# Kernel optimization log

Hardware: AMD Instinct MI355X
Metric: run time of the kernel (lower is better)

Reference implementation:

```python
import jax, jax.numpy as jnp
import numpy as np

BIGINT = 1e10

def sinusoidal_embed(pos, dim):
    # SinusoidalPositionEmbedding: interleaved sin/cos, matches torch reshape order
    idx = jnp.arange(dim // 2, dtype=jnp.float32)
    freq = jnp.power(10000.0, -2.0 * idx / dim)
    ang = pos.astype(jnp.float32)[:, None] * freq[None, :]          # [N, d/2]
    emb = jnp.stack([jnp.sin(ang), jnp.cos(ang)], axis=-1)          # [N, d/2, 2]
    return emb.reshape(pos.shape[0], dim)

def dihedral(a, b, c, d):
    # standard signed dihedral angle of four points, [...,3] -> [...]
    u1, u2, u3 = b - a, c - b, d - c
    n1 = jnp.cross(u1, u2)
    n2 = jnp.cross(u2, u3)
    u2n = u2 / (jnp.linalg.norm(u2, axis=-1, keepdims=True) + 1e-12)
    m = jnp.cross(n1, u2n)
    x = jnp.sum(n1 * n2, axis=-1)
    y = jnp.sum(m * n2, axis=-1)
    return jnp.arctan2(y, x)

def knn_edges(X, Seg, bid, k):
    # faithful dense formulation of _construct_knn: pairwise min-over-channel-pair
    # distance, masked by (same bid) & (same Seg), then smallest-k per row.
    N = X.shape[0]
    rule = (bid[:, None] == bid[None, :]) & (Seg[:, None] == Seg[None, :])  # [N,N]
    sq = jnp.sum(X * X, axis=-1)                                   # [N,C]
    dot = jnp.einsum('icd,jed->icje', X, X)                        # [N,C,N,C]
    d2 = sq[:, :, None, None] + sq[None, None, :, :] - 2.0 * dot   # [N,C,N,C]
    dmin = jnp.sqrt(jnp.maximum(jnp.min(d2, axis=(1, 3)), 0.0))    # [N,N]
    dist = jnp.where(rule, dmin, BIGINT)
    neg_vals, dst = jax.lax.top_k(-dist, k)                        # smallest-k
    dnb = -neg_vals                                                # [N,k]
    src = jnp.broadcast_to(jnp.arange(N)[:, None], (N, k))
    valid = (dnb < BIGINT).reshape(-1)                             # [N*k]
    dst = dst.reshape(-1)
    src = src.reshape(-1)
    # torch compacts invalid edges (dynamic shape); we pad them with -1 + mask
    edges = jnp.stack([jnp.where(valid, dst, -1), jnp.where(valid, src, -1)])
    return edges, valid

def pairwise_dihedrals(X, dst, src):
    # inter-residue dihedrals on backbone atoms, channels = [N, CA, C, O]
    ir_phi = dihedral(X[dst, 2], X[src, 0], X[src, 1], X[src, 2])  # C_i, N_j, CA_j, C_j
    ir_psi = dihedral(X[dst, 0], X[dst, 1], X[dst, 2], X[src, 0])  # N_i, CA_i, C_i, N_j
    return jnp.stack([ir_phi, ir_psi], axis=-1)                    # [E, 2]

def setup_inputs() -> dict:
    key = jax.random.key(0)
    ks = jax.random.split(key, 8)
    N, C, E, NUM_AA, NUM_ID = 3000, 4, 64, 21, 2
    X = jax.random.normal(ks[0], (N, C, 3), dtype=jnp.float32) * 10.0
    S = jax.random.randint(ks[1], (N,), 0, NUM_AA)
    RP = jax.random.randint(ks[2], (N,), 0, 1000)
    ID = jax.random.randint(ks[3], (N,), 0, NUM_ID)
    Seg = jax.random.randint(ks[4], (N,), 0, 2)
    bid = jnp.sort(jax.random.randint(ks[5], (N,), 0, 8))
    res_embed = jax.random.normal(ks[6], (NUM_AA, E), dtype=jnp.float32)
    id_embed = jax.random.normal(ks[7], (NUM_ID, E), dtype=jnp.float32)
    return {"X": X, "S": S, "RP": RP, "ID": ID, "Seg": Seg, "bid": bid,
            "res_embed": res_embed, "id_embed": id_embed, "k_neighbors": 10}

def reference(X, S, RP, ID, Seg, bid, res_embed, id_embed, k_neighbors):
    # node features: [residue embedding, positional + chain-id embedding]
    res_h = res_embed[S]                                           # [N,E]
    rp_h = sinusoidal_embed(RP, res_embed.shape[1]) + id_embed[ID] # [N,E]
    H = jnp.concatenate([res_h, rp_h], axis=-1)                    # [N,2E]
    edges, valid = knn_edges(X, Seg, bid, k_neighbors)             # [2,N*k], [N*k]
    dst = jnp.maximum(edges[0], 0)
    src = jnp.maximum(edges[1], 0)
    edge_attr = pairwise_dihedrals(X, dst, src)                    # [N*k,2]
    edge_attr = jnp.where(valid[:, None], edge_attr, 0.0)
    return H, edges, edge_attr, valid
```

## Files before the change

kernel.cpp:

```cpp
#include <hip/hip_runtime.h>
#include <math.h>

#define TOPK 10
#define WAVE 64
#define MAX_N 3072

__device__ __forceinline__ void cross3(const float* a, const float* b, float* o) {
    o[0] = a[1] * b[2] - a[2] * b[1];
    o[1] = a[2] * b[0] - a[0] * b[2];
    o[2] = a[0] * b[1] - a[1] * b[0];
}
__device__ __forceinline__ float dot3(const float* a, const float* b) {
    return a[0] * b[0] + a[1] * b[1] + a[2] * b[2];
}

__device__ float dihedral4(const float* a, const float* b, const float* c, const float* d) {
    float u1[3], u2[3], u3[3];
    #pragma unroll
    for (int t = 0; t < 3; t++) {
        u1[t] = b[t] - a[t];
        u2[t] = c[t] - b[t];
        u3[t] = d[t] - c[t];
    }
    float n1[3], n2[3];
    cross3(u1, u2, n1);
    cross3(u2, u3, n2);
    float nrm = sqrtf(dot3(u2, u2)) + 1e-12f;
    float u2n[3] = {u2[0] / nrm, u2[1] / nrm, u2[2] / nrm};
    float m[3];
    cross3(n1, u2n, m);
    float x = dot3(n1, n2);
    float y = dot3(m, n2);
    return atan2f(y, x);
}

__global__ void node_feat_kernel(const float* __restrict__ res_embed,
                                 const float* __restrict__ id_embed,
                                 const int* __restrict__ S,
                                 const int* __restrict__ RP,
                                 const int* __restrict__ ID,
                                 float* __restrict__ H,
                                 int N, int E) {
    int idx = blockIdx.x * blockDim.x + threadIdx.x;
    if (idx >= N * E) return;
    int n = idx / E;
    int e = idx - n * E;
    float* Hrow = H + (size_t)n * 2 * E;
    Hrow[e] = res_embed[S[n] * E + e];
    if (e < E / 2) {
        int half = e;
        float freq = powf(10000.0f, -2.0f * (float)half / (float)E);
        float ang = (float)RP[n] * freq;
        const float* idrow = id_embed + ID[n] * E;
        Hrow[E + 2 * half + 0] = sinf(ang) + idrow[2 * half + 0];
        Hrow[E + 2 * half + 1] = cosf(ang) + idrow[2 * half + 1];
    }
}

__global__ __launch_bounds__(WAVE) void knn_wave_kernel(
    const float* __restrict__ X,
    const int* __restrict__ Seg,
    const int* __restrict__ bid,
    float* __restrict__ out_e0,
    float* __restrict__ out_e1,
    float* __restrict__ out_attr,
    float* __restrict__ out_valid,
    int N) {
    __shared__ int cand[MAX_N];

    const int i = blockIdx.x;
    const int lane = threadIdx.x;

    float xi[4][3], sqi[4];
    #pragma unroll
    for (int c = 0; c < 4; c++) {
        xi[c][0] = X[(i * 4 + c) * 3 + 0];
        xi[c][1] = X[(i * 4 + c) * 3 + 1];
        xi[c][2] = X[(i * 4 + c) * 3 + 2];
        sqi[c] = xi[c][0] * xi[c][0] + xi[c][1] * xi[c][1] + xi[c][2] * xi[c][2];
    }
    const int bi = bid[i];
    const int si = Seg[i];

    int count = 0;
    for (int j = lane; j < N; j += WAVE) {
        bool ok = (bid[j] == bi) && (Seg[j] == si);
        unsigned long long mask = __ballot(ok);
        if (ok) {
            int pos = count + __popcll(mask & ((1ull << lane) - 1ull));
            cand[pos] = j;
        }
        count += (int)__popcll(mask);
    }
    __syncthreads();

    const unsigned long long EMPTY = ~0ull;
    unsigned long long best[TOPK];
    #pragma unroll
    for (int t = 0; t < TOPK; t++) best[t] = EMPTY;
    unsigned long long curmax = EMPTY;

    for (int t = lane; t < count; t += WAVE) {
        int j = cand[t];
        float xj[4][3], sqj[4];
        #pragma unroll
        for (int c = 0; c < 4; c++) {
            xj[c][0] = X[(j * 4 + c) * 3 + 0];
            xj[c][1] = X[(j * 4 + c) * 3 + 1];
            xj[c][2] = X[(j * 4 + c) * 3 + 2];
            sqj[c] = xj[c][0] * xj[c][0] + xj[c][1] * xj[c][1] + xj[c][2] * xj[c][2];
        }
        float bestd2 = 3.4e38f;
        #pragma unroll
        for (int c = 0; c < 4; c++) {
            #pragma unroll
            for (int e = 0; e < 4; e++) {
                float dp = xi[c][0] * xj[e][0] + xi[c][1] * xj[e][1] + xi[c][2] * xj[e][2];
                float d2 = (sqi[c] + sqj[e]) - 2.0f * dp;
                bestd2 = fminf(bestd2, d2);
            }
        }
        float dist = sqrtf(fmaxf(bestd2, 0.0f));
        unsigned long long key =
            ((unsigned long long)__float_as_uint(dist) << 32) | (unsigned)j;

        if (key < curmax) {
            bool done = false;
            #pragma unroll
            for (int u = 0; u < TOPK; u++) {
                bool hit = (!done) && (best[u] == curmax);
                if (hit) { best[u] = key; done = true; }
            }
            curmax = best[0];
            #pragma unroll
            for (int u = 1; u < TOPK; u++) curmax = (best[u] > curmax) ? best[u] : curmax;
        }
    }

    unsigned long long mywin = EMPTY;
    for (int t = 0; t < TOPK; t++) {
        unsigned long long m = best[0];
        #pragma unroll
        for (int u = 1; u < TOPK; u++) m = (best[u] < m) ? best[u] : m;
        #pragma unroll
        for (int off = 32; off > 0; off >>= 1) {
            unsigned long long o = __shfl_xor(m, off, WAVE);
            m = (o < m) ? o : m;
        }
        if (lane == t) mywin = m;
        #pragma unroll
        for (int u = 0; u < TOPK; u++) {
            if (best[u] == m) best[u] = EMPTY;
        }
    }

    if (lane < TOPK) {
        int j = (int)(mywin & 0xffffffffu);
        bool valid = (mywin != EMPTY);
        int e = i * TOPK + lane;

        out_e0[e] = valid ? (float)j : -1.0f;
        out_e1[e] = valid ? (float)i : -1.0f;
        out_valid[e] = valid ? 1.0f : 0.0f;

        float phi = 0.0f, psi = 0.0f;
        if (valid) {
            float xj[4][3];
            #pragma unroll
            for (int c = 0; c < 4; c++) {
                xj[c][0] = X[(j * 4 + c) * 3 + 0];
                xj[c][1] = X[(j * 4 + c) * 3 + 1];
                xj[c][2] = X[(j * 4 + c) * 3 + 2];
            }
            phi = dihedral4(xj[2], xi[0], xi[1], xi[2]);
            psi = dihedral4(xj[0], xj[1], xj[2], xi[0]);
        }
        out_attr[e * 2 + 0] = phi;
        out_attr[e * 2 + 1] = psi;
    }
}

extern "C" void kernel_launch(void* const* d_in, const int* in_sizes, int n_in,
                              void* d_out, int out_size, void* d_ws, size_t ws_size,
                              hipStream_t stream) {
    const float* X = (const float*)d_in[0];
    const int* S = (const int*)d_in[1];
    const int* RP = (const int*)d_in[2];
    const int* ID = (const int*)d_in[3];
    const int* Seg = (const int*)d_in[4];
    const int* bid = (const int*)d_in[5];
    const float* res_embed = (const float*)d_in[6];
    const float* id_embed = (const float*)d_in[7];

    const int N = in_sizes[1];
    const int E = 64;

    float* out = (float*)d_out;
    float* H = out;
    float* e0 = H + (size_t)N * 2 * E;
    float* e1 = e0 + (size_t)N * TOPK;
    float* attr = e1 + (size_t)N * TOPK;
    float* validp = attr + (size_t)N * TOPK * 2;

    int total = N * E;
    hipLaunchKernelGGL(node_feat_kernel, dim3((total + 255) / 256), dim3(256), 0, stream,
                       res_embed, id_embed, S, RP, ID, H, N, E);
    hipLaunchKernelGGL(knn_wave_kernel, dim3(N), dim3(WAVE), 0, stream,
                       X, Seg, bid, e0, e1, attr, validp, N);
}
```

Measured before the change: 98.41 us.

## Precompute per-group candidate lists once instead of per-row filtering

Adds a small kernel that builds compacted candidate index lists for each (bid, Seg) group in workspace, so each row's kNN block reads its group list instead of scanning all N entries of bid/Seg. Row coordinates are also loaded as three float4 vectors. This removes the per-row O(N) filter pass and its shared-memory buffer, at the cost of an extra launch and a hardcoded assumption of at most 8 bids and 2 segments.

```diff
diff --git a/kernel.cpp b/kernel.cpp
--- a/kernel.cpp
+++ b/kernel.cpp
@@ -3,7 +3,7 @@
 
 #define TOPK 10
 #define WAVE 64
-#define MAX_N 3072
+#define NGROUPS 16
 
 __device__ __forceinline__ void cross3(const float* a, const float* b, float* o) {
     o[0] = a[1] * b[2] - a[2] * b[1];
@@ -32,6 +32,17 @@
     float x = dot3(n1, n2);
     float y = dot3(m, n2);
     return atan2f(y, x);
+}
+
+__device__ __forceinline__ void load_xrow(const float4* __restrict__ X4, int j,
+                                          float xj[4][3]) {
+    float4 a = X4[j * 3 + 0];
+    float4 b = X4[j * 3 + 1];
+    float4 c = X4[j * 3 + 2];
+    xj[0][0] = a.x; xj[0][1] = a.y; xj[0][2] = a.z;
+    xj[1][0] = a.w; xj[1][1] = b.x; xj[1][2] = b.y;
+    xj[2][0] = b.z; xj[2][1] = b.w; xj[2][2] = c.x;
+    xj[3][0] = c.y; xj[3][1] = c.z; xj[3][2] = c.w;
 }
 
 __global__ void node_feat_kernel(const float* __restrict__ res_embed,
@@ -57,42 +68,55 @@
     }
 }
 
-__global__ __launch_bounds__(WAVE) void knn_wave_kernel(
+__global__ __launch_bounds__(WAVE) void build_groups_kernel(
+    const int* __restrict__ Seg,
+    const int* __restrict__ bid,
+    int* __restrict__ lists,
+    int* __restrict__ counts,
+    int N) {
+    const int g = blockIdx.x;
+    const int gb = g >> 1;
+    const int gs = g & 1;
+    const int lane = threadIdx.x;
+
+    int cnt = 0;
+    int* list = lists + (size_t)g * N;
+    for (int j = lane; j < N; j += WAVE) {
+        bool ok = (bid[j] == gb) && (Seg[j] == gs);
+        unsigned long long mask = __ballot(ok);
+        if (ok) {
+            int pos = cnt + __popcll(mask & ((1ull << lane) - 1ull));
+            list[pos] = j;
+        }
+        cnt += (int)__popcll(mask);
+    }
+    if (lane == 0) counts[g] = cnt;
+}
+
+__global__ __launch_bounds__(WAVE) void knn_rows_kernel(
     const float* __restrict__ X,
     const int* __restrict__ Seg,
     const int* __restrict__ bid,
+    const int* __restrict__ lists,
+    const int* __restrict__ counts,
     float* __restrict__ out_e0,
     float* __restrict__ out_e1,
     float* __restrict__ out_attr,
     float* __restrict__ out_valid,
     int N) {
-    __shared__ int cand[MAX_N];
-
     const int i = blockIdx.x;
     const int lane = threadIdx.x;
+    const float4* X4 = (const float4*)X;
 
     float xi[4][3], sqi[4];
+    load_xrow(X4, i, xi);
     #pragma unroll
-    for (int c = 0; c < 4; c++) {
-        xi[c][0] = X[(i * 4 + c) * 3 + 0];
-        xi[c][1] = X[(i * 4 + c) * 3 + 1];
-        xi[c][2] = X[(i * 4 + c) * 3 + 2];
+    for (int c = 0; c < 4; c++)
         sqi[c] = xi[c][0] * xi[c][0] + xi[c][1] * xi[c][1] + xi[c][2] * xi[c][2];
-    }
-    const int bi = bid[i];
-    const int si = Seg[i];
-
-    int count = 0;
-    for (int j = lane; j < N; j += WAVE) {
-        bool ok = (bid[j] == bi) && (Seg[j] == si);
-        unsigned long long mask = __ballot(ok);
-        if (ok) {
-            int pos = count + __popcll(mask & ((1ull << lane) - 1ull));
-            cand[pos] = j;
-        }
-        count += (int)__popcll(mask);
-    }
-    __syncthreads();
+
+    const int g = (bid[i] << 1) | Seg[i];
+    const int cnt = counts[g];
+    const int* list = lists + (size_t)g * N;
 
     const unsigned long long EMPTY = ~0ull;
     unsigned long long best[TOPK];
@@ -100,16 +124,14 @@
     for (int t = 0; t < TOPK; t++) best[t] = EMPTY;
     unsigned long long curmax = EMPTY;
 
-    for (int t = lane; t < count; t += WAVE) {
-        int j = cand[t];
+    for (int t = lane; t < cnt; t += WAVE) {
+        int j = list[t];
         float xj[4][3], sqj[4];
-        #pragma unroll
-        for (int c = 0; c < 4; c++) {
-            xj[c][0] = X[(j * 4 + c) * 3 + 0];
-            xj[c][1] = X[(j * 4 + c) * 3 + 1];
-            xj[c][2] = X[(j * 4 + c) * 3 + 2];
+        load_xrow(X4, j, xj);
+        #pragma unroll
+        for (int c = 0; c < 4; c++)
             sqj[c] = xj[c][0] * xj[c][0] + xj[c][1] * xj[c][1] + xj[c][2] * xj[c][2];
-        }
+
         float bestd2 = 3.4e38f;
         #pragma unroll
         for (int c = 0; c < 4; c++) {
@@ -166,12 +188,7 @@
         float phi = 0.0f, psi = 0.0f;
         if (valid) {
             float xj[4][3];
-            #pragma unroll
-            for (int c = 0; c < 4; c++) {
-                xj[c][0] = X[(j * 4 + c) * 3 + 0];
-                xj[c][1] = X[(j * 4 + c) * 3 + 1];
-                xj[c][2] = X[(j * 4 + c) * 3 + 2];
-            }
+            load_xrow(X4, j, xj);
             phi = dihedral4(xj[2], xi[0], xi[1], xi[2]);
             psi = dihedral4(xj[0], xj[1], xj[2], xi[0]);
         }
@@ -202,9 +219,14 @@
     float* attr = e1 + (size_t)N * TOPK;
     float* validp = attr + (size_t)N * TOPK * 2;
 
+    int* counts = (int*)d_ws;
+    int* lists = (int*)((char*)d_ws + 256);
+
     int total = N * E;
     hipLaunchKernelGGL(node_feat_kernel, dim3((total + 255) / 256), dim3(256), 0, stream,
                        res_embed, id_embed, S, RP, ID, H, N, E);
-    hipLaunchKernelGGL(knn_wave_kernel, dim3(N), dim3(WAVE), 0, stream,
-                       X, Seg, bid, e0, e1, attr, validp, N);
-}
+    hipLaunchKernelGGL(build_groups_kernel, dim3(NGROUPS), dim3(WAVE), 0, stream,
+                       Seg, bid, lists, counts, N);
+    hipLaunchKernelGGL(knn_rows_kernel, dim3(N), dim3(WAVE), 0, stream,
+                       X, Seg, bid, lists, counts, e0, e1, attr, validp, N);
+}
```

Result: slower. 109.8 us (+11.5%).
